# Optimization experiments

Hardware: AMD Instinct MI355X
Metric: run time of the kernel (lower is better)

Reference implementation:

```python
import jax, jax.numpy as jnp
import numpy as np

NUM_E = 1024
E_DIM = 64
BETA = 0.5


def setup_inputs() -> dict:
    key = jax.random.key(0)
    k1, k2 = jax.random.split(key)
    z_e = jax.random.normal(k1, (32, E_DIM, 64, 64), dtype=jnp.float32)  # [B, C, H, W]
    codebook = jax.random.uniform(k2, (NUM_E, E_DIM), dtype=jnp.float32,
                                  minval=-1.0 / NUM_E, maxval=1.0 / NUM_E)
    return {"z_e": z_e, "codebook": codebook}


def reference(z_e, codebook):
    B, C, H, W = z_e.shape
    sg = jax.lax.stop_gradient
    z = jnp.transpose(z_e, (0, 2, 3, 1))            # [B, H, W, C]
    zf = z.reshape(-1, C)                           # [N, C]
    # squared L2 distances via ||z||^2 + ||e||^2 - 2 z.e  -> [N, num_e]
    d = (jnp.sum(zf * zf, axis=1, keepdims=True)
         + jnp.sum(codebook * codebook, axis=1)
         - 2.0 * jnp.matmul(zf, codebook.T))
    idx = jnp.argmin(d, axis=1)                     # [N]
    z_q = codebook[idx].reshape(z.shape)            # gather instead of one-hot matmul
    loss = jnp.mean((sg(z_q) - z) ** 2) + BETA * jnp.mean((z_q - sg(z)) ** 2)
    z_q_st = z + sg(z_q - z)                        # straight-through
    # code usage histogram == mean of one-hot encodings
    counts = jnp.zeros((NUM_E,), dtype=z.dtype).at[idx].add(1.0)
    e_mean = counts / idx.shape[0]
    perplexity = jnp.exp(-jnp.sum(e_mean * jnp.log(e_mean + 1e-10)))
    z_q_out = jnp.transpose(z_q_st, (0, 3, 1, 2))   # back to [B, C, H, W]
    return (z_q_out, loss, sg(perplexity), idx.reshape(B, H, W))
```

## Files before the change

### kernel.cpp

```cpp
#include <hip/hip_runtime.h>
#include <math.h>

#define NUM_E   1024
#define ZQ_ELEM 8388608
#define AGRID   256
#define MAXC    7
#define OQCAP   512

typedef short bf16x8 __attribute__((ext_vector_type(8)));
typedef float f32x16 __attribute__((ext_vector_type(16)));

__device__ inline unsigned short rne_bf16(float v) {
    unsigned u = __float_as_uint(v);
    return (unsigned short)((u + 0x7FFFu + ((u >> 16) & 1u)) >> 16);
}

__global__ __launch_bounds__(256) void vq_prep(const float* __restrict__ cb,
                                               float* __restrict__ ee,
                                               unsigned short* __restrict__ ehi)
{
    int j = blockIdx.x * 256 + threadIdx.x;
    const float* r = cb + (size_t)j * 64;
    float v[64];
#pragma unroll
    for (int k = 0; k < 64; ++k) v[k] = r[k];
    float a = 0.f;
#pragma unroll
    for (int k = 0; k < 64; ++k) a = fmaf(v[k], v[k], a);
    ee[j] = a;

    int nt = j >> 5, jc = j & 31;
#pragma unroll
    for (int kt = 0; kt < 4; ++kt)
#pragma unroll
        for (int h = 0; h < 2; ++h) {
            bf16x8 vh;
#pragma unroll
            for (int i = 0; i < 8; ++i)
                vh[i] = (short)rne_bf16(v[kt * 16 + h * 8 + i]);
            *(bf16x8*)(ehi + ((size_t)(nt * 4 + kt) * 64 + h * 32 + jc) * 8) = vh;
        }
}

__device__ inline unsigned long long key_regs(const float* vv, float zz, float eej,
                                              const float* cb, int j)
{
    const float4* cr = (const float4*)(cb + ((size_t)j << 6));
    float a = 0.f;
#pragma unroll
    for (int q = 0; q < 16; ++q) {
        float4 c4 = cr[q];
        a = fmaf(vv[4 * q + 0], c4.x, a);
        a = fmaf(vv[4 * q + 1], c4.y, a);
        a = fmaf(vv[4 * q + 2], c4.z, a);
        a = fmaf(vv[4 * q + 3], c4.w, a);
    }
    float t1 = zz + eej;
    float d  = fmaf(-2.f, a, t1);
    return ((unsigned long long)__float_as_uint(d) << 32) | (unsigned long long)j;
}

__device__ inline unsigned long long key_glob(const float* zb, float zz, float eej,
                                              const float* cb, int pl, int j)
{
    const float4* cr = (const float4*)(cb + ((size_t)j << 6));
    float a = 0.f;
#pragma unroll
    for (int q = 0; q < 16; ++q) {
        float4 c4 = cr[q];
        a = fmaf(zb[(size_t)(4 * q + 0) * 4096 + pl], c4.x, a);
        a = fmaf(zb[(size_t)(4 * q + 1) * 4096 + pl], c4.y, a);
        a = fmaf(zb[(size_t)(4 * q + 2) * 4096 + pl], c4.z, a);
        a = fmaf(zb[(size_t)(4 * q + 3) * 4096 + pl], c4.w, a);
    }
    float t1 = zz + eej;
    float d  = fmaf(-2.f, a, t1);
    return ((unsigned long long)__float_as_uint(d) << 32) | (unsigned long long)j;
}

__global__ __launch_bounds__(512, 2) void vq_argmin(
    const float* __restrict__ z, const float* __restrict__ cb,
    const unsigned short* __restrict__ ehi, const float* __restrict__ ee,
    float* __restrict__ idx_f, int* __restrict__ counts,
    float* __restrict__ zq, double* __restrict__ partials)
{
    __shared__ bf16x8 bB[8192];
    __shared__ float  eeL[1024];
    __shared__ float  zzsL[512];
    __shared__ float  wp[512];
    __shared__ unsigned long long best[512];
    __shared__ unsigned short cand[512 * MAXC];
    __shared__ unsigned int ccnt[512];
    __shared__ unsigned int oq[OQCAP];
    __shared__ unsigned int oqcnt, gflow;
    __shared__ double wsum[8];

    const int tid  = threadIdx.x;
    const int g    = blockIdx.x;
    const int lane = tid & 63, wv = tid >> 6;
    const size_t zoff = ((size_t)(g >> 3) << 18) + (size_t)((g & 7) << 9);
    const float* zb = z + zoff;

    best[tid] = 0xFFFFFFFFFFFFFFFFull;
    ccnt[tid] = 0;
    if (tid == 0) { oqcnt = 0; gflow = 0; }
    eeL[tid]       = ee[tid];
    eeL[tid + 512] = ee[tid + 512];

    {
        const uint4* src = (const uint4*)ehi;
        uint4* dst = (uint4*)bB;
#pragma unroll
        for (int pass = 0; pass < 4; ++pass) {
            uint4 a = src[pass * 2048 + tid];
            uint4 b = src[pass * 2048 + 512 + tid];
            uint4 c = src[pass * 2048 + 1024 + tid];
            uint4 d = src[pass * 2048 + 1536 + tid];
            dst[pass * 2048 + tid] = a;
            dst[pass * 2048 + 512 + tid] = b;
            dst[pass * 2048 + 1024 + tid] = c;
            dst[pass * 2048 + 1536 + tid] = d;
        }
    }

    float vv[64];
#pragma unroll
    for (int k = 0; k < 64; ++k) vv[k] = zb[(size_t)k * 4096 + tid];
    float zz;
    {
        float a = 0.f;
#pragma unroll
        for (int k = 0; k < 64; ++k) a = fmaf(vv[k], vv[k], a);
        zz = a; zzsL[tid] = a;
    }

    bf16x8 ah0[4], ah1[4];
    {
        int h = lane >> 5;
#pragma unroll
        for (int g2 = 0; g2 < 2; ++g2) {
            int pl = wv * 64 + g2 * 32 + (lane & 31);
            float s1 = 0.f, sd = 0.f;
#pragma unroll
            for (int kt = 0; kt < 4; ++kt)
#pragma unroll
                for (int i = 0; i < 8; ++i) {
                    int k = kt * 16 + h * 8 + i;
                    float x = zb[(size_t)k * 4096 + pl];
                    unsigned short hb = rne_bf16(x);
                    float hf = __uint_as_float((unsigned)hb << 16);
                    if (g2 == 0) ah0[kt][i] = (short)hb; else ah1[kt][i] = (short)hb;
                    s1 += fabsf(x);
                    sd += fabsf(x - hf);
                }
            s1 += __shfl_xor(s1, 32);
            sd += __shfl_xor(sd, 32);
            if (lane < 32) wp[pl] = 4.f * (s1 * 1.907e-6f + sd * 9.785e-4f) + 1.4e-4f;
        }
    }
    __syncthreads();

    float m0[16], m1[16];
#pragma unroll
    for (int r = 0; r < 16; ++r) { m0[r] = 3.4e38f; m1[r] = 3.4e38f; }

#pragma unroll 2
    for (int nt = 0; nt < 32; ++nt) {
        bf16x8 b0 = bB[(nt * 4 + 0) * 64 + lane];
        bf16x8 b1 = bB[(nt * 4 + 1) * 64 + lane];
        bf16x8 b2 = bB[(nt * 4 + 2) * 64 + lane];
        bf16x8 b3 = bB[(nt * 4 + 3) * 64 + lane];
        float eA = eeL[nt * 32 + (lane & 31)];
        f32x16 a0, a1;
#pragma unroll
        for (int r = 0; r < 16; ++r) { a0[r] = 0.f; a1[r] = 0.f; }
        a0 = __builtin_amdgcn_mfma_f32_32x32x16_bf16(ah0[0], b0, a0, 0, 0, 0);
        a1 = __builtin_amdgcn_mfma_f32_32x32x16_bf16(ah1[0], b0, a1, 0, 0, 0);
        a0 = __builtin_amdgcn_mfma_f32_32x32x16_bf16(ah0[1], b1, a0, 0, 0, 0);
        a1 = __builtin_amdgcn_mfma_f32_32x32x16_bf16(ah1[1], b1, a1, 0, 0, 0);
        a0 = __builtin_amdgcn_mfma_f32_32x32x16_bf16(ah0[2], b2, a0, 0, 0, 0);
        a1 = __builtin_amdgcn_mfma_f32_32x32x16_bf16(ah1[2], b2, a1, 0, 0, 0);
        a0 = __builtin_amdgcn_mfma_f32_32x32x16_bf16(ah0[3], b3, a0, 0, 0, 0);
        a1 = __builtin_amdgcn_mfma_f32_32x32x16_bf16(ah1[3], b3, a1, 0, 0, 0);
#pragma unroll
        for (int r = 0; r < 16; ++r) {
            m0[r] = fminf(m0[r], fmaf(-2.f, a0[r], eA));
            m1[r] = fminf(m1[r], fmaf(-2.f, a1[r], eA));
        }
    }
#pragma unroll
    for (int r = 0; r < 16; ++r) {
        for (int d2 = 1; d2 <= 16; d2 <<= 1) {
            m0[r] = fminf(m0[r], __shfl_xor(m0[r], d2));
            m1[r] = fminf(m1[r], __shfl_xor(m1[r], d2));
        }
        int row = 4 * (lane >> 5) + (r & 3) + 8 * (r >> 2);
        m0[r] += wp[wv * 64 + row];
        m1[r] += wp[wv * 64 + 32 + row];
    }

#define ENQ(PL, JJ) do {                                                  \
    unsigned _s = atomicAdd(&ccnt[PL], 1u);                               \
    if (_s < MAXC) cand[(PL) * MAXC + _s] = (unsigned short)(JJ);         \
    else { unsigned _o = atomicAdd(&oqcnt, 1u);                           \
           if (_o < OQCAP) oq[_o] = ((unsigned)(PL) << 16) | (JJ);        \
           else gflow = 1; }                                              \
} while (0)

#pragma unroll 1
    for (int nt = 0; nt < 32; ++nt) {
        bf16x8 b0 = bB[(nt * 4 + 0) * 64 + lane];
        bf16x8 b1 = bB[(nt * 4 + 1) * 64 + lane];
        bf16x8 b2 = bB[(nt * 4 + 2) * 64 + lane];
        bf16x8 b3 = bB[(nt * 4 + 3) * 64 + lane];
        float eA = eeL[nt * 32 + (lane & 31)];
        f32x16 a0, a1;
#pragma unroll
        for (int r = 0; r < 16; ++r) { a0[r] = 0.f; a1[r] = 0.f; }
        a0 = __builtin_amdgcn_mfma_f32_32x32x16_bf16(ah0[0], b0, a0, 0, 0, 0);
        a1 = __builtin_amdgcn_mfma_f32_32x32x16_bf16(ah1[0], b0, a1, 0, 0, 0);
        a0 = __builtin_amdgcn_mfma_f32_32x32x16_bf16(ah0[1], b1, a0, 0, 0, 0);
        a1 = __builtin_amdgcn_mfma_f32_32x32x16_bf16(ah1[1], b1, a1, 0, 0, 0);
        a0 = __builtin_amdgcn_mfma_f32_32x32x16_bf16(ah0[2], b2, a0, 0, 0, 0);
        a1 = __builtin_amdgcn_mfma_f32_32x32x16_bf16(ah1[2], b2, a1, 0, 0, 0);
        a0 = __builtin_amdgcn_mfma_f32_32x32x16_bf16(ah0[3], b3, a0, 0, 0, 0);
        a1 = __builtin_amdgcn_mfma_f32_32x32x16_bf16(ah1[3], b3, a1, 0, 0, 0);
        unsigned jj = (unsigned)(nt * 32 + (lane & 31));
#pragma unroll
        for (int r = 0; r < 16; ++r) {
            int row = 4 * (lane >> 5) + (r & 3) + 8 * (r >> 2);
            bool h0 = fmaf(-2.f, a0[r], eA) <= m0[r];
            if (__any(h0)) { if (h0) { int pl = wv * 64 + row;      ENQ(pl, jj); } }
            bool h1 = fmaf(-2.f, a1[r], eA) <= m1[r];
            if (__any(h1)) { if (h1) { int pl = wv * 64 + 32 + row; ENQ(pl, jj); } }
        }
    }
    __syncthreads();

    if (gflow) {
        unsigned long long bk = 0xFFFFFFFFFFFFFFFFull;
        for (int j = 0; j < NUM_E; ++j) {
            unsigned long long k2 = key_regs(vv, zz, eeL[j], cb, j);
            if (k2 < bk) bk = k2;
        }
        best[tid] = bk;
    } else {
        int n = (int)ccnt[tid]; if (n > MAXC) n = MAXC;
        unsigned long long bk = 0xFFFFFFFFFFFFFFFFull;
        for (int e = 0; e < n; ++e) {
            int j = (int)cand[tid * MAXC + e];
            unsigned long long k2 = key_regs(vv, zz, eeL[j], cb, j);
            if (k2 < bk) bk = k2;
        }
        atomicMin(&best[tid], bk);
        int no = (int)oqcnt; if (no > OQCAP) no = OQCAP;
        for (int e = tid; e < no; e += 512) {
            unsigned u = oq[e];
            int pl = (int)(u >> 16), j = (int)(u & 0xFFFFu);
            atomicMin(&best[pl], key_glob(zb, zzsL[pl], eeL[j], cb, pl, j));
        }
    }
    __syncthreads();

    {
        int bi = (int)(best[tid] & 0xFFFFFFFFull);
        idx_f[(size_t)g * 512 + tid] = (float)bi;
        atomicAdd(&counts[bi], 1);
        const float* crow = cb + ((size_t)bi << 6);
        float* zqp = zq + zoff + tid;
        double ls = 0.0;
#pragma unroll
        for (int c = 0; c < 64; ++c) {
            float q = crow[c];
            float t = q - vv[c];
            zqp[(size_t)c * 4096] = vv[c] + t;
            ls += (double)t * t;
        }
#pragma unroll
        for (int off = 32; off > 0; off >>= 1) ls += __shfl_down(ls, off);
        if (lane == 0) wsum[wv] = ls;
    }
    __syncthreads();
    if (tid == 0) {
        double s = 0.0;
#pragma unroll
        for (int i = 0; i < 8; ++i) s += wsum[i];
        partials[g] = s;
    }
}

__global__ __launch_bounds__(256) void vq_final(
    const int* __restrict__ counts, const double* __restrict__ partials,
    float* __restrict__ scalars)
{
    __shared__ double sh[256];
    __shared__ double sl[256];
    int t = threadIdx.x;
    double s = 0.0;
    for (int j = t; j < NUM_E; j += 256) {
        float em   = (float)counts[j] * (1.0f / 131072.0f);
        float term = em * logf(em + 1e-10f);
        s += (double)term;
    }
    double l = 0.0;
#pragma unroll
    for (int j = 0; j < AGRID / 256; ++j) l += partials[j * 256 + t];
    sh[t] = s;
    sl[t] = l;
    __syncthreads();
    for (int off = 128; off > 0; off >>= 1) {
        if (t < off) { sh[t] += sh[t + off]; sl[t] += sl[t + off]; }
        __syncthreads();
    }
    if (t == 0) {
        float mm = (float)(sl[0] / 8388608.0);
        scalars[0] = mm + 0.5f * mm;
        scalars[1] = expf(-(float)sh[0]);
    }
}

extern "C" void kernel_launch(void* const* d_in, const int* in_sizes, int n_in,
                              void* d_out, int out_size, void* d_ws, size_t ws_size,
                              hipStream_t stream)
{
    const float* z  = (const float*)d_in[0];
    const float* cb = (const float*)d_in[1];
    float* out     = (float*)d_out;
    float* zq      = out;
    float* scalars = out + ZQ_ELEM;
    float* idx_f   = out + ZQ_ELEM + 2;

    int*            counts   = (int*)d_ws;
    double*         partials = (double*)((char*)d_ws + 4096);
    float*          ee       = (float*)((char*)d_ws + 12288);
    unsigned short* ehi      = (unsigned short*)((char*)d_ws + 16384);

    hipMemsetAsync(d_ws, 0, 4096, stream);
    vq_prep  <<<4,     256, 0, stream>>>(cb, ee, ehi);
    vq_argmin<<<AGRID, 512, 0, stream>>>(z, cb, ehi, ee, idx_f, counts, zq, partials);
    vq_final <<<1,     256, 0, stream>>>(counts, partials, scalars);
}
```

Baseline: 122.8 us.

## Use 1024-thread blocks with one 32-row MFMA tile per wave and vectorized epilogue

Doubles the block to 1024 threads so each wave handles a single 32-point MFMA tile instead of two. This halves per-thread accumulators and drops the 64-float z register cache; rescoring now rereads z from global memory. The epilogue is rewritten to use float4 loads and stores across all 1024 threads via a shared index buffer. The aim is to cut register pressure, raise latency hiding and coalesce the z_q writes, at the cost of extra global reads during candidate rescoring.

```diff
diff --git a/kernel.cpp b/kernel.cpp
--- a/kernel.cpp
+++ b/kernel.cpp
@@ -40,24 +40,6 @@
                 vh[i] = (short)rne_bf16(v[kt * 16 + h * 8 + i]);
             *(bf16x8*)(ehi + ((size_t)(nt * 4 + kt) * 64 + h * 32 + jc) * 8) = vh;
         }
-}
-
-__device__ inline unsigned long long key_regs(const float* vv, float zz, float eej,
-                                              const float* cb, int j)
-{
-    const float4* cr = (const float4*)(cb + ((size_t)j << 6));
-    float a = 0.f;
-#pragma unroll
-    for (int q = 0; q < 16; ++q) {
-        float4 c4 = cr[q];
-        a = fmaf(vv[4 * q + 0], c4.x, a);
-        a = fmaf(vv[4 * q + 1], c4.y, a);
-        a = fmaf(vv[4 * q + 2], c4.z, a);
-        a = fmaf(vv[4 * q + 3], c4.w, a);
-    }
-    float t1 = zz + eej;
-    float d  = fmaf(-2.f, a, t1);
-    return ((unsigned long long)__float_as_uint(d) << 32) | (unsigned long long)j;
 }
 
 __device__ inline unsigned long long key_glob(const float* zb, float zz, float eej,
@@ -78,7 +60,7 @@
     return ((unsigned long long)__float_as_uint(d) << 32) | (unsigned long long)j;
 }
 
-__global__ __launch_bounds__(512, 2) void vq_argmin(
+__global__ __launch_bounds__(1024, 4) void vq_argmin(
     const float* __restrict__ z, const float* __restrict__ cb,
     const unsigned short* __restrict__ ehi, const float* __restrict__ ee,
     float* __restrict__ idx_f, int* __restrict__ counts,
@@ -86,14 +68,15 @@
 {
     __shared__ bf16x8 bB[8192];
     __shared__ float  eeL[1024];
-    __shared__ float  zzsL[512];
+    __shared__ float  zzs[512];
     __shared__ float  wp[512];
     __shared__ unsigned long long best[512];
     __shared__ unsigned short cand[512 * MAXC];
     __shared__ unsigned int ccnt[512];
     __shared__ unsigned int oq[OQCAP];
+    __shared__ int ibuf[512];
     __shared__ unsigned int oqcnt, gflow;
-    __shared__ double wsum[8];
+    __shared__ double wsum[16];
 
     const int tid  = threadIdx.x;
     const int g    = blockIdx.x;
@@ -101,68 +84,53 @@
     const size_t zoff = ((size_t)(g >> 3) << 18) + (size_t)((g & 7) << 9);
     const float* zb = z + zoff;
 
-    best[tid] = 0xFFFFFFFFFFFFFFFFull;
-    ccnt[tid] = 0;
+    eeL[tid] = ee[tid];
+    if (tid < 512) { best[tid] = 0xFFFFFFFFFFFFFFFFull; ccnt[tid] = 0; }
     if (tid == 0) { oqcnt = 0; gflow = 0; }
-    eeL[tid]       = ee[tid];
-    eeL[tid + 512] = ee[tid + 512];
-
     {
         const uint4* src = (const uint4*)ehi;
         uint4* dst = (uint4*)bB;
 #pragma unroll
-        for (int pass = 0; pass < 4; ++pass) {
-            uint4 a = src[pass * 2048 + tid];
-            uint4 b = src[pass * 2048 + 512 + tid];
-            uint4 c = src[pass * 2048 + 1024 + tid];
-            uint4 d = src[pass * 2048 + 1536 + tid];
-            dst[pass * 2048 + tid] = a;
-            dst[pass * 2048 + 512 + tid] = b;
-            dst[pass * 2048 + 1024 + tid] = c;
-            dst[pass * 2048 + 1536 + tid] = d;
-        }
-    }
-
-    float vv[64];
-#pragma unroll
-    for (int k = 0; k < 64; ++k) vv[k] = zb[(size_t)k * 4096 + tid];
-    float zz;
-    {
+        for (int i = 0; i < 8; ++i)
+            dst[i * 1024 + tid] = src[i * 1024 + tid];
+    }
+
+    if (tid < 512) {
         float a = 0.f;
 #pragma unroll
-        for (int k = 0; k < 64; ++k) a = fmaf(vv[k], vv[k], a);
-        zz = a; zzsL[tid] = a;
-    }
-
-    bf16x8 ah0[4], ah1[4];
+        for (int k = 0; k < 64; ++k) {
+            float v = zb[(size_t)k * 4096 + tid];
+            a = fmaf(v, v, a);
+        }
+        zzs[tid] = a;
+    }
+
+    bf16x8 ah[4];
     {
         int h = lane >> 5;
-#pragma unroll
-        for (int g2 = 0; g2 < 2; ++g2) {
-            int pl = wv * 64 + g2 * 32 + (lane & 31);
-            float s1 = 0.f, sd = 0.f;
-#pragma unroll
-            for (int kt = 0; kt < 4; ++kt)
-#pragma unroll
-                for (int i = 0; i < 8; ++i) {
-                    int k = kt * 16 + h * 8 + i;
-                    float x = zb[(size_t)k * 4096 + pl];
-                    unsigned short hb = rne_bf16(x);
-                    float hf = __uint_as_float((unsigned)hb << 16);
-                    if (g2 == 0) ah0[kt][i] = (short)hb; else ah1[kt][i] = (short)hb;
-                    s1 += fabsf(x);
-                    sd += fabsf(x - hf);
-                }
-            s1 += __shfl_xor(s1, 32);
-            sd += __shfl_xor(sd, 32);
-            if (lane < 32) wp[pl] = 4.f * (s1 * 1.907e-6f + sd * 9.785e-4f) + 1.4e-4f;
-        }
-    }
-    __syncthreads();
-
-    float m0[16], m1[16];
-#pragma unroll
-    for (int r = 0; r < 16; ++r) { m0[r] = 3.4e38f; m1[r] = 3.4e38f; }
+        int pl = wv * 32 + (lane & 31);
+        float s1 = 0.f, sd = 0.f;
+#pragma unroll
+        for (int kt = 0; kt < 4; ++kt)
+#pragma unroll
+            for (int i = 0; i < 8; ++i) {
+                int k = kt * 16 + h * 8 + i;
+                float x = zb[(size_t)k * 4096 + pl];
+                unsigned short hb = rne_bf16(x);
+                float hf = __uint_as_float((unsigned)hb << 16);
+                ah[kt][i] = (short)hb;
+                s1 += fabsf(x);
+                sd += fabsf(x - hf);
+            }
+        s1 += __shfl_xor(s1, 32);
+        sd += __shfl_xor(sd, 32);
+        if (lane < 32) wp[pl] = 4.f * (s1 * 1.907e-6f + sd * 9.785e-4f) + 1.4e-4f;
+    }
+    __syncthreads();
+
+    float m[16];
+#pragma unroll
+    for (int r = 0; r < 16; ++r) m[r] = 3.4e38f;
 
 #pragma unroll 2
     for (int nt = 0; nt < 32; ++nt) {
@@ -171,32 +139,21 @@
         bf16x8 b2 = bB[(nt * 4 + 2) * 64 + lane];
         bf16x8 b3 = bB[(nt * 4 + 3) * 64 + lane];
         float eA = eeL[nt * 32 + (lane & 31)];
-        f32x16 a0, a1;
-#pragma unroll
-        for (int r = 0; r < 16; ++r) { a0[r] = 0.f; a1[r] = 0.f; }
-        a0 = __builtin_amdgcn_mfma_f32_32x32x16_bf16(ah0[0], b0, a0, 0, 0, 0);
-        a1 = __builtin_amdgcn_mfma_f32_32x32x16_bf16(ah1[0], b0, a1, 0, 0, 0);
-        a0 = __builtin_amdgcn_mfma_f32_32x32x16_bf16(ah0[1], b1, a0, 0, 0, 0);
-        a1 = __builtin_amdgcn_mfma_f32_32x32x16_bf16(ah1[1], b1, a1, 0, 0, 0);
-        a0 = __builtin_amdgcn_mfma_f32_32x32x16_bf16(ah0[2], b2, a0, 0, 0, 0);
-        a1 = __builtin_amdgcn_mfma_f32_32x32x16_bf16(ah1[2], b2, a1, 0, 0, 0);
-        a0 = __builtin_amdgcn_mfma_f32_32x32x16_bf16(ah0[3], b3, a0, 0, 0, 0);
-        a1 = __builtin_amdgcn_mfma_f32_32x32x16_bf16(ah1[3], b3, a1, 0, 0, 0);
-#pragma unroll
-        for (int r = 0; r < 16; ++r) {
-            m0[r] = fminf(m0[r], fmaf(-2.f, a0[r], eA));
-            m1[r] = fminf(m1[r], fmaf(-2.f, a1[r], eA));
-        }
+        f32x16 acc;
+#pragma unroll
+        for (int r = 0; r < 16; ++r) acc[r] = 0.f;
+        acc = __builtin_amdgcn_mfma_f32_32x32x16_bf16(ah[0], b0, acc, 0, 0, 0);
+        acc = __builtin_amdgcn_mfma_f32_32x32x16_bf16(ah[1], b1, acc, 0, 0, 0);
+        acc = __builtin_amdgcn_mfma_f32_32x32x16_bf16(ah[2], b2, acc, 0, 0, 0);
+        acc = __builtin_amdgcn_mfma_f32_32x32x16_bf16(ah[3], b3, acc, 0, 0, 0);
+#pragma unroll
+        for (int r = 0; r < 16; ++r) m[r] = fminf(m[r], fmaf(-2.f, acc[r], eA));
     }
 #pragma unroll
     for (int r = 0; r < 16; ++r) {
-        for (int d2 = 1; d2 <= 16; d2 <<= 1) {
-            m0[r] = fminf(m0[r], __shfl_xor(m0[r], d2));
-            m1[r] = fminf(m1[r], __shfl_xor(m1[r], d2));
-        }
-        int row = 4 * (lane >> 5) + (r & 3) + 8 * (r >> 2);
-        m0[r] += wp[wv * 64 + row];
-        m1[r] += wp[wv * 64 + 32 + row];
+        for (int d2 = 1; d2 <= 16; d2 <<= 1)
+            m[r] = fminf(m[r], __shfl_xor(m[r], d2));
+        m[r] += wp[wv * 32 + 4 * (lane >> 5) + (r & 3) + 8 * (r >> 2)];
     }
 
 #define ENQ(PL, JJ) do {                                                  \
@@ -214,67 +171,81 @@
         bf16x8 b2 = bB[(nt * 4 + 2) * 64 + lane];
         bf16x8 b3 = bB[(nt * 4 + 3) * 64 + lane];
         float eA = eeL[nt * 32 + (lane & 31)];
-        f32x16 a0, a1;
-#pragma unroll
-        for (int r = 0; r < 16; ++r) { a0[r] = 0.f; a1[r] = 0.f; }
-        a0 = __builtin_amdgcn_mfma_f32_32x32x16_bf16(ah0[0], b0, a0, 0, 0, 0);
-        a1 = __builtin_amdgcn_mfma_f32_32x32x16_bf16(ah1[0], b0, a1, 0, 0, 0);
-        a0 = __builtin_amdgcn_mfma_f32_32x32x16_bf16(ah0[1], b1, a0, 0, 0, 0);
-        a1 = __builtin_amdgcn_mfma_f32_32x32x16_bf16(ah1[1], b1, a1, 0, 0, 0);
-        a0 = __builtin_amdgcn_mfma_f32_32x32x16_bf16(ah0[2], b2, a0, 0, 0, 0);
-        a1 = __builtin_amdgcn_mfma_f32_32x32x16_bf16(ah1[2], b2, a1, 0, 0, 0);
-        a0 = __builtin_amdgcn_mfma_f32_32x32x16_bf16(ah0[3], b3, a0, 0, 0, 0);
-        a1 = __builtin_amdgcn_mfma_f32_32x32x16_bf16(ah1[3], b3, a1, 0, 0, 0);
+        f32x16 acc;
+#pragma unroll
+        for (int r = 0; r < 16; ++r) acc[r] = 0.f;
+        acc = __builtin_amdgcn_mfma_f32_32x32x16_bf16(ah[0], b0, acc, 0, 0, 0);
+        acc = __builtin_amdgcn_mfma_f32_32x32x16_bf16(ah[1], b1, acc, 0, 0, 0);
+        acc = __builtin_amdgcn_mfma_f32_32x32x16_bf16(ah[2], b2, acc, 0, 0, 0);
+        acc = __builtin_amdgcn_mfma_f32_32x32x16_bf16(ah[3], b3, acc, 0, 0, 0);
         unsigned jj = (unsigned)(nt * 32 + (lane & 31));
 #pragma unroll
         for (int r = 0; r < 16; ++r) {
-            int row = 4 * (lane >> 5) + (r & 3) + 8 * (r >> 2);
-            bool h0 = fmaf(-2.f, a0[r], eA) <= m0[r];
-            if (__any(h0)) { if (h0) { int pl = wv * 64 + row;      ENQ(pl, jj); } }
-            bool h1 = fmaf(-2.f, a1[r], eA) <= m1[r];
-            if (__any(h1)) { if (h1) { int pl = wv * 64 + 32 + row; ENQ(pl, jj); } }
+            bool hit = fmaf(-2.f, acc[r], eA) <= m[r];
+            if (__any(hit)) {
+                if (hit) {
+                    int pl = wv * 32 + 4 * (lane >> 5) + (r & 3) + 8 * (r >> 2);
+                    ENQ(pl, jj);
+                }
+            }
         }
     }
     __syncthreads();
 
     if (gflow) {
-        unsigned long long bk = 0xFFFFFFFFFFFFFFFFull;
-        for (int j = 0; j < NUM_E; ++j) {
-            unsigned long long k2 = key_regs(vv, zz, eeL[j], cb, j);
-            if (k2 < bk) bk = k2;
-        }
-        best[tid] = bk;
+        if (tid < 512) {
+            unsigned long long bk = 0xFFFFFFFFFFFFFFFFull;
+            for (int j = 0; j < NUM_E; ++j) {
+                unsigned long long k2 = key_glob(zb, zzs[tid], eeL[j], cb, tid, j);
+                if (k2 < bk) bk = k2;
+            }
+            best[tid] = bk;
+        }
     } else {
-        int n = (int)ccnt[tid]; if (n > MAXC) n = MAXC;
-        unsigned long long bk = 0xFFFFFFFFFFFFFFFFull;
-        for (int e = 0; e < n; ++e) {
-            int j = (int)cand[tid * MAXC + e];
-            unsigned long long k2 = key_regs(vv, zz, eeL[j], cb, j);
-            if (k2 < bk) bk = k2;
-        }
-        atomicMin(&best[tid], bk);
+        if (tid < 512) {
+            int n = (int)ccnt[tid]; if (n > MAXC) n = MAXC;
+            unsigned long long bk = 0xFFFFFFFFFFFFFFFFull;
+            for (int e = 0; e < n; ++e) {
+                int j = (int)cand[tid * MAXC + e];
+                unsigned long long k2 = key_glob(zb, zzs[tid], eeL[j], cb, tid, j);
+                if (k2 < bk) bk = k2;
+            }
+            atomicMin(&best[tid], bk);
+        }
         int no = (int)oqcnt; if (no > OQCAP) no = OQCAP;
-        for (int e = tid; e < no; e += 512) {
+        for (int e = tid; e < no; e += 1024) {
             unsigned u = oq[e];
             int pl = (int)(u >> 16), j = (int)(u & 0xFFFFu);
-            atomicMin(&best[pl], key_glob(zb, zzsL[pl], eeL[j], cb, pl, j));
-        }
-    }
-    __syncthreads();
-
-    {
+            atomicMin(&best[pl], key_glob(zb, zzs[pl], eeL[j], cb, pl, j));
+        }
+    }
+    __syncthreads();
+    if (tid < 512) {
         int bi = (int)(best[tid] & 0xFFFFFFFFull);
+        ibuf[tid] = bi;
         idx_f[(size_t)g * 512 + tid] = (float)bi;
         atomicAdd(&counts[bi], 1);
-        const float* crow = cb + ((size_t)bi << 6);
-        float* zqp = zq + zoff + tid;
+    }
+    __syncthreads();
+
+    {
+        int w4 = tid & 127, c8 = (tid >> 7) * 8;
+        const float4* zb4 = (const float4*)zb;
+        float4* zq4 = (float4*)(zq + zoff);
+        size_t b0 = (size_t)ibuf[w4 * 4 + 0] << 6;
+        size_t b1 = (size_t)ibuf[w4 * 4 + 1] << 6;
+        size_t b2 = (size_t)ibuf[w4 * 4 + 2] << 6;
+        size_t b3 = (size_t)ibuf[w4 * 4 + 3] << 6;
         double ls = 0.0;
 #pragma unroll
-        for (int c = 0; c < 64; ++c) {
-            float q = crow[c];
-            float t = q - vv[c];
-            zqp[(size_t)c * 4096] = vv[c] + t;
-            ls += (double)t * t;
+        for (int i = 0; i < 8; ++i) {
+            int c = c8 + i;
+            float4 zv = zb4[(size_t)c * 1024 + w4];
+            float q0 = cb[b0 + c], q1 = cb[b1 + c], q2 = cb[b2 + c], q3 = cb[b3 + c];
+            float t0 = q0 - zv.x, t1 = q1 - zv.y, t2 = q2 - zv.z, t3 = q3 - zv.w;
+            zq4[(size_t)c * 1024 + w4] =
+                make_float4(zv.x + t0, zv.y + t1, zv.z + t2, zv.w + t3);
+            ls += (double)t0 * t0 + (double)t1 * t1 + (double)t2 * t2 + (double)t3 * t3;
         }
 #pragma unroll
         for (int off = 32; off > 0; off >>= 1) ls += __shfl_down(ls, off);
@@ -284,7 +255,7 @@
     if (tid == 0) {
         double s = 0.0;
 #pragma unroll
-        for (int i = 0; i < 8; ++i) s += wsum[i];
+        for (int i = 0; i < 16; ++i) s += wsum[i];
         partials[g] = s;
     }
 }
@@ -337,6 +308,6 @@
 
     hipMemsetAsync(d_ws, 0, 4096, stream);
     vq_prep  <<<4,     256, 0, stream>>>(cb, ee, ehi);
-    vq_argmin<<<AGRID, 512, 0, stream>>>(z, cb, ehi, ee, idx_f, counts, zq, partials);
+    vq_argmin<<<AGRID, 1024, 0, stream>>>(z, cb, ehi, ee, idx_f, counts, zq, partials);
     vq_final <<<1,     256, 0, stream>>>(counts, partials, scalars);
 }
```

After: 114.1 us. 1.08x faster.
